# Kernel optimization log

Hardware: AMD Instinct MI355X
Metric: run time of the kernel (lower is better)

The kernel has to match this reference:

```python
import jax, jax.numpy as jnp
import numpy as np

EPS = 1e-5
NEG_SLOPE = 0.1


def conv_bn_lrelu(x, w, g, b, rm, rv):
    # 1x1 conv (no bias) + BatchNorm (inference, running stats) + LeakyReLU(0.1)
    # x: [B,C,H,W], w: [O,C]
    y = jnp.einsum('bchw,oc->bohw', x, w)
    scale = g / jnp.sqrt(rv + EPS)
    y = y * scale[None, :, None, None] + (b - rm * scale)[None, :, None, None]
    return jnp.where(y >= 0, y, NEG_SLOPE * y)


def setup_inputs() -> dict:
    key = jax.random.key(0)
    ks = jax.random.split(key, 16)
    B, C, H1, W1, H2, W2 = 4, 256, 32, 32, 64, 64
    C8 = C // 8
    inp = {
        'x1': jax.random.normal(ks[0], (B, C, H1, W1), jnp.float32),
        'x2': jax.random.normal(ks[1], (B, C, H2, W2), jnp.float32),
        'wq': jax.random.normal(ks[2], (C8, C), jnp.float32) * 0.05,
        'wk': jax.random.normal(ks[3], (C8, C), jnp.float32) * 0.05,
        'wv': jax.random.normal(ks[4], (C, C), jnp.float32) * 0.05,
        'gq': jnp.ones((C8,), jnp.float32), 'bq': jnp.zeros((C8,), jnp.float32),
        'mq': jax.random.normal(ks[5], (C8,), jnp.float32) * 0.1,
        'vq': jax.random.uniform(ks[6], (C8,), jnp.float32, 0.5, 1.5),
        'gk': jnp.ones((C8,), jnp.float32), 'bk': jnp.zeros((C8,), jnp.float32),
        'mk': jax.random.normal(ks[7], (C8,), jnp.float32) * 0.1,
        'vk': jax.random.uniform(ks[8], (C8,), jnp.float32, 0.5, 1.5),
        'gv': jnp.ones((C,), jnp.float32), 'bv': jnp.zeros((C,), jnp.float32),
        'mv': jax.random.normal(ks[9], (C,), jnp.float32) * 0.1,
        'vv': jax.random.uniform(ks[10], (C,), jnp.float32, 0.5, 1.5),
        'gamma': jnp.full((1,), 0.5, jnp.float32),
    }
    return inp


def reference(x1, x2, wq, wk, wv, gq, bq, mq, vq, gk, bk, mk, vk, gv, bv, mv, vv, gamma):
    B, C, H2, W2 = x2.shape
    # bilinear upsample x1 to x2's spatial size (align_corners=False == half-pixel)
    x1u = jax.image.resize(x1, (B, C, H2, W2), method='bilinear')
    N = H2 * W2
    q = conv_bn_lrelu(x1u, wq, gq, bq, mq, vq).reshape(B, -1, N)  # [B,C8,N]
    k = conv_bn_lrelu(x2, wk, gk, bk, mk, vk).reshape(B, -1, N)   # [B,C8,N]
    v = conv_bn_lrelu(x2, wv, gv, bv, mv, vv).reshape(B, -1, N)   # [B,C,N]
    energy = jnp.einsum('bdm,bdn->bmn', q, k)                      # [B,N,N]
    attn = jax.nn.softmax(energy, axis=-1)
    out = jnp.einsum('bcn,bmn->bcm', v, attn).reshape(B, C, H2, W2)
    return gamma[0] * out + x1u
```

## Files before the change

kernel.cpp:

```cpp
#include <hip/hip_runtime.h>

#define B_ 4
#define C_ 256
#define N_ 4096
#define LOG2E 1.4426950408889634f

typedef short short8 __attribute__((ext_vector_type(8)));
typedef short short4_ __attribute__((ext_vector_type(4)));
typedef float float4v __attribute__((ext_vector_type(4)));
typedef unsigned int uint2v __attribute__((ext_vector_type(2)));
typedef unsigned int u32;

__device__ inline unsigned short f2b(float x){
  unsigned u = __builtin_bit_cast(unsigned, x);
  u = u + 0x7FFFu + ((u >> 16) & 1u);
  return (unsigned short)(u >> 16);
}

__device__ inline u32 cvtpk(float lo, float hi){
  u32 r; asm("v_cvt_pk_bf16_f32 %0, %1, %2" : "=v"(r) : "v"(lo), "v"(hi)); return r;
}

__device__ inline void gload16(const void* g, void* l){
  __builtin_amdgcn_global_load_lds((const __attribute__((address_space(1))) u32*)g,
                                   (__attribute__((address_space(3))) u32*)l, 16, 0, 0);
}

__global__ void fold_w_kernel(const float* __restrict__ wq, const float* __restrict__ wk,
    const float* __restrict__ wv,
    const float* gq, const float* bq, const float* mq, const float* vq,
    const float* gk, const float* bk, const float* mk, const float* vk,
    const float* gv, const float* bv, const float* mv, const float* vv,
    unsigned short* wqb, unsigned short* wkb, unsigned short* wvb,
    float* biasq, float* biask, float* biasv){
  int i = blockIdx.x*256 + threadIdx.x;
  int o = i >> 8;
  float sv = gv[o]*rsqrtf(vv[o]+1e-5f);
  wvb[i] = f2b(wv[i]*sv);
  if (i < 32*256){
    int oq = i >> 8;
    float sq = gq[oq]*rsqrtf(vq[oq]+1e-5f);
    wqb[i] = f2b(wq[i]*sq*LOG2E);
    float sk = gk[oq]*rsqrtf(vk[oq]+1e-5f);
    wkb[i] = f2b(wk[i]*sk);
  }
  if (i < 256) biasv[i] = bv[i] - mv[i]*(gv[i]*rsqrtf(vv[i]+1e-5f));
  if (i < 32){
    biasq[i] = (bq[i] - mq[i]*(gq[i]*rsqrtf(vq[i]+1e-5f)))*LOG2E;
    biask[i] = bk[i] - mk[i]*(gk[i]*rsqrtf(vk[i]+1e-5f));
  }
}

__global__ __launch_bounds__(256, 2)
void pre_kernel(const float* __restrict__ x1, const float* __restrict__ x2,
                const unsigned short* __restrict__ wqb,
                const unsigned short* __restrict__ wkb,
                const unsigned short* __restrict__ wvb,
                const float* __restrict__ biasq, const float* __restrict__ biask,
                const float* __restrict__ biasv,
                float* __restrict__ x1u,
                unsigned short* __restrict__ Qb, unsigned short* __restrict__ Kb,
                unsigned short* __restrict__ Vb){
  __shared__ unsigned short xt[64*260];
  int b = blockIdx.y;
  int t = threadIdx.x;
  int lane = t&63, w = t>>6, l15 = lane&15, g = lane>>4;

  if (blockIdx.z == 0){
    int y = blockIdx.x;
    float fy = 0.5f*y - 0.25f;
    float y0f = floorf(fy); float wy = fy - y0f;
    int y0 = max(0,min(31,(int)y0f)), y1 = max(0,min(31,(int)y0f+1));
    int x = t & 63, cg = t >> 6;
    float fx = 0.5f*x - 0.25f;
    float x0f = floorf(fx); float wx = fx - x0f;
    int x0 = max(0,min(31,(int)x0f)), x1i = max(0,min(31,(int)x0f+1));
    #pragma unroll 8
    for (int i=0;i<64;i++){
      int c = cg + i*4;
      const float* s0 = x1 + ((size_t)(b*C_ + c)*32 + y0)*32;
      const float* s1 = x1 + ((size_t)(b*C_ + c)*32 + y1)*32;
      float v00=s0[x0], v01=s0[x1i], v10=s1[x0], v11=s1[x1i];
      float v0 = v00 + wx*(v01-v00), v1 = v10 + wx*(v11-v10);
      float val = v0 + wy*(v1-v0);
      x1u[(size_t)(b*C_ + c)*N_ + y*64 + x] = val;
      xt[x*260 + c] = f2b(val);
    }
    __syncthreads();
    const unsigned short* arow = xt + (w*16+l15)*260 + g*8;
    short8 a[8];
    #pragma unroll
    for (int kk=0;kk<8;kk++){
      short4_ lo = *(const short4_*)(arow + kk*32);
      short4_ hi = *(const short4_*)(arow + kk*32 + 4);
      short8 af;
      af[0]=lo[0];af[1]=lo[1];af[2]=lo[2];af[3]=lo[3];
      af[4]=hi[0];af[5]=hi[1];af[6]=hi[2];af[7]=hi[3];
      a[kk]=af;
    }
    #pragma unroll
    for (int ot=0; ot<2; ot++){
      int o = ot*16 + l15;
      const unsigned short* wrow = wqb + o*C_ + g*8;
      float4v acc = {0.f,0.f,0.f,0.f};
      #pragma unroll
      for (int kk=0;kk<8;kk++){
        short8 bf = *(const short8*)(wrow + kk*32);
        acc = __builtin_amdgcn_mfma_f32_16x16x32_bf16(a[kk], bf, acc, 0,0,0);
      }
      float bs = biasq[o];
      #pragma unroll
      for (int r=0;r<4;r++){
        float yv = acc[r] + bs;
        yv = yv >= 0.f ? yv : 0.1f*yv;
        int m = y*64 + w*16 + g*4 + r;
        Qb[(size_t)(b*N_+m)*32 + o] = f2b(yv);
      }
    }
  } else {
    int n0 = blockIdx.x*64;
    int n = t & 63, cg = t >> 6;
    #pragma unroll 8
    for (int i=0;i<64;i++){
      int c = cg + i*4;
      float v = x2[(size_t)(b*C_ + c)*N_ + n0 + n];
      xt[n*260 + c] = f2b(v);
    }
    __syncthreads();
    const unsigned short* arow = xt + (w*16+l15)*260 + g*8;
    short8 a[8];
    #pragma unroll
    for (int kk=0;kk<8;kk++){
      short4_ lo = *(const short4_*)(arow + kk*32);
      short4_ hi = *(const short4_*)(arow + kk*32 + 4);
      short8 af;
      af[0]=lo[0];af[1]=lo[1];af[2]=lo[2];af[3]=lo[3];
      af[4]=hi[0];af[5]=hi[1];af[6]=hi[2];af[7]=hi[3];
      a[kk]=af;
    }
    if (blockIdx.z == 1){
      #pragma unroll
      for (int ot=0; ot<2; ot++){
        int o = ot*16 + l15;
        const unsigned short* wrow = wkb + o*C_ + g*8;
        float4v acc = {0.f,0.f,0.f,0.f};
        #pragma unroll
        for (int kk=0;kk<8;kk++){
          short8 bf = *(const short8*)(wrow + kk*32);
          acc = __builtin_amdgcn_mfma_f32_16x16x32_bf16(a[kk], bf, acc, 0,0,0);
        }
        float bs = biask[o];
        #pragma unroll
        for (int r=0;r<4;r++){
          float yv = acc[r] + bs;
          yv = yv >= 0.f ? yv : 0.1f*yv;
          int m = n0 + w*16 + g*4 + r;
          Kb[(size_t)(b*N_+m)*32 + o] = f2b(yv);
        }
      }
    }
    int obase = (blockIdx.z == 1) ? 0 : 8;
    #pragma unroll
    for (int ot=0; ot<8; ot++){
      int o = (obase + ot)*16 + l15;
      const unsigned short* wrow = wvb + (size_t)o*C_ + g*8;
      float4v acc = {0.f,0.f,0.f,0.f};
      #pragma unroll
      for (int kk=0;kk<8;kk++){
        short8 bf = *(const short8*)(wrow + kk*32);
        acc = __builtin_amdgcn_mfma_f32_16x16x32_bf16(a[kk], bf, acc, 0,0,0);
      }
      float bs = biasv[o];
      #pragma unroll
      for (int r=0;r<4;r++){
        float yv = acc[r] + bs;
        yv = yv >= 0.f ? yv : 0.1f*yv;
        int m = n0 + w*16 + g*4 + r;
        Vb[(size_t)(b*C_ + o)*N_ + m] = f2b(yv);
      }
    }
  }
}

__global__ __launch_bounds__(512, 2)
void attn_kernel(const unsigned short* __restrict__ Qb,
                 const unsigned short* __restrict__ Kb,
                 const unsigned short* __restrict__ Vb,
                 const float* __restrict__ x1u,
                 const float* __restrict__ gamma_p,
                 float* __restrict__ out){
  __shared__ __align__(16) char smem[82720];
  int* flagsB = (int*)(smem + 81920);
  float* sclB = (float*)(smem + 81952);
  float* lst  = (float*)(smem + 82464);

  int wg = blockIdx.y*64 + blockIdx.x;
  int id = (wg & 7)*32 + (wg >> 3);
  int b = id >> 6, mblk = id & 63;
  int t = threadIdx.x, lane = t & 63, w = t >> 6;
  int l15 = lane & 15, g = lane >> 4;
  int swz = (l15 & 7) << 4;
  int cq = w & 3, ks = w >> 2;

  short8 qf{};
  if (w < 4)
    qf = *(const short8*)(Qb + (size_t)(b*N_ + mblk*64 + w*16 + l15)*32 + g*8);

  float4v acc[4][4];
  #pragma unroll
  for (int mt=0;mt<4;mt++)
    #pragma unroll
    for (int ct=0;ct<4;ct++) acc[mt][ct] = (float4v){0.f,0.f,0.f,0.f};
  float mrow = -1e30f, lrun = 0.f;
  const float4v zero4 = {0.f,0.f,0.f,0.f};

  size_t goff[4]; int loff[4];
  #pragma unroll
  for (int j=0;j<4;j++){
    int i = j*512 + t;
    int c = i >> 3, jj = i & 7;
    loff[j] = i*16;
    goff[j] = (size_t)(b*C_ + c)*(N_*2) + ((size_t)((jj ^ (c & 7)) << 4));
  }
  const char* Vbyte = (const char*)Vb;
  const short* kbase = (const short*)Kb + (size_t)(b*N_ + l15)*32 + g*8;

  auto stageV = [&](int tt, char* buf){
    const char* src = Vbyte + tt*128;
    #pragma unroll
    for (int j=0;j<4;j++) gload16(src + goff[j], buf + loff[j]);
  };
  auto loadK = [&](short8 (&kf)[4], int tt){
    const short* kp = kbase + (size_t)tt*64*32;
    #pragma unroll
    for (int j=0;j<4;j++) kf[j] = *(const short8*)(kp + j*512);
  };

  auto softmax_step = [&](const short8 (&kf)[4], int pdst){
    float4v s[4];
    #pragma unroll
    for (int j=0;j<4;j++)
      s[j] = __builtin_amdgcn_mfma_f32_16x16x32_bf16(kf[j], qf, zero4, 0, 0, 0);
    float tmax = fmaxf(fmaxf(fmaxf(s[0][0],s[0][1]),fmaxf(s[0][2],s[0][3])),
               fmaxf(fmaxf(fmaxf(s[1][0],s[1][1]),fmaxf(s[1][2],s[1][3])),
               fmaxf(fmaxf(fmaxf(s[2][0],s[2][1]),fmaxf(s[2][2],s[2][3])),
                     fmaxf(fmaxf(s[3][0],s[3][1]),fmaxf(s[3][2],s[3][3])))));
    int trig = __any((tmax > mrow + 8.f) ? 1 : 0) ? 1 : 0;
    if (lane == 0) flagsB[pdst*4 + w] = trig;
    if (trig){
      float tm = fmaxf(tmax, __shfl_xor(tmax, 16));
      tm = fmaxf(tm, __shfl_xor(tm, 32));
      float mnew = fmaxf(mrow, tm);
      float sc = exp2f(mrow - mnew);
      mrow = mnew; lrun *= sc;
      if (lane < 16) sclB[pdst*64 + w*16 + l15] = sc;
    }
    char* pw = smem + 65536 + pdst*8192 + w*2048 + l15*128;
    #pragma unroll
    for (int j=0;j<4;j++){
      float p0 = exp2f(s[j][0]-mrow), p1 = exp2f(s[j][1]-mrow);
      float p2 = exp2f(s[j][2]-mrow), p3 = exp2f(s[j][3]-mrow);
      lrun += (p0+p1)+(p2+p3);
      u32 lo = cvtpk(p0, p1);
      u32 hi = cvtpk(p2, p3);
      *(uint2v*)(pw + ((j*32 + g*8) ^ swz)) = (uint2v){lo, hi};
    }
  };

  auto body = [&](int tt, short8 (&kC)[4], short8 (&kN)[4]){
    int pp = tt & 1, vb = tt & 1;
    char* vbc = smem + vb*32768;
    if (tt < 63) stageV(tt+1, smem + (vb^1)*32768);
    if (w < 4){
      loadK(kN, (tt+2) & 63);
      if (tt < 63) softmax_step(kC, pp ^ 1);
    }
    #pragma unroll
    for (int mt=0;mt<4;mt++){
      if (flagsB[pp*4 + mt]){
        float4v sv = *(float4v*)(sclB + pp*64 + mt*16 + g*4);
        #pragma unroll
        for (int ct=0;ct<4;ct++){
          acc[mt][ct][0]*=sv[0]; acc[mt][ct][1]*=sv[1];
          acc[mt][ct][2]*=sv[2]; acc[mt][ct][3]*=sv[3];
        }
      }
    }
    int ko = (ks*64 + g*16) ^ swz;
    short8 pa[4], vf[4];
    #pragma unroll
    for (int mt=0;mt<4;mt++)
      pa[mt] = *(const short8*)(smem + 65536 + pp*8192 + mt*2048 + l15*128 + ko);
    #pragma unroll
    for (int ct=0;ct<4;ct++)
      vf[ct] = *(const short8*)(vbc + (cq*64 + ct*16 + l15)*128 + ko);
    __builtin_amdgcn_s_setprio(1);
    #pragma unroll
    for (int mt=0;mt<4;mt++)
      #pragma unroll
      for (int ct=0;ct<4;ct++)
        acc[mt][ct] = __builtin_amdgcn_mfma_f32_16x16x32_bf16(pa[mt], vf[ct], acc[mt][ct], 0, 0, 0);
    __builtin_amdgcn_s_setprio(0);
    __syncthreads();
  };

  short8 kA[4], kB[4];
  stageV(0, smem);
  if (w < 4){
    short8 k0[4];
    loadK(k0, 0);
    softmax_step(k0, 0);
    loadK(kA, 1);
  }
  __syncthreads();

  for (int tt=0; tt<64; tt+=2){
    body(tt,   kA, kB);
    body(tt+1, kB, kA);
  }

  if (w < 4){
    lrun += __shfl_xor(lrun, 16);
    lrun += __shfl_xor(lrun, 32);
    if (lane < 16) lst[w*16 + l15] = lrun;
  }
  float* cb = (float*)smem + cq*4160;
  if (ks == 1){
    #pragma unroll
    for (int mt=0;mt<4;mt++)
      #pragma unroll
      for (int ct=0;ct<4;ct++)
        #pragma unroll
        for (int r=0;r<4;r++)
          cb[(mt*16 + g*4 + r)*65 + ct*16 + l15] = acc[mt][ct][r];
  }
  __syncthreads();
  if (ks == 0){
    float4v lv[4];
    #pragma unroll
    for (int mt=0;mt<4;mt++) lv[mt] = *(float4v*)(lst + mt*16 + g*4);
    #pragma unroll
    for (int mt=0;mt<4;mt++)
      #pragma unroll
      for (int ct=0;ct<4;ct++)
        #pragma unroll
        for (int r=0;r<4;r++){
          int idx = (mt*16 + g*4 + r)*65 + ct*16 + l15;
          cb[idx] = (acc[mt][ct][r] + cb[idx]) / lv[mt][r];
        }
  }
  __syncthreads();
  float gm = gamma_p[0];
  const float* xr = x1u + (size_t)(b*C_ + cq*64 + ks*32)*N_ + mblk*64;
  float* orow = out + (size_t)(b*C_ + cq*64 + ks*32)*N_ + mblk*64;
  #pragma unroll 8
  for (int i=0; i<32; i++){
    int c_l = ks*32 + i;
    float v = cb[lane*65 + c_l];
    orow[(size_t)i*N_ + lane] = gm*v + xr[(size_t)i*N_ + lane];
  }
}

extern "C" void kernel_launch(void* const* d_in, const int* in_sizes, int n_in,
                              void* d_out, int out_size, void* d_ws, size_t ws_size,
                              hipStream_t stream){
  (void)in_sizes; (void)n_in; (void)out_size; (void)ws_size;
  const float* x1 = (const float*)d_in[0];
  const float* x2 = (const float*)d_in[1];
  const float* wq = (const float*)d_in[2];
  const float* wk = (const float*)d_in[3];
  const float* wv = (const float*)d_in[4];
  const float* gq = (const float*)d_in[5];
  const float* bq = (const float*)d_in[6];
  const float* mq = (const float*)d_in[7];
  const float* vq = (const float*)d_in[8];
  const float* gk = (const float*)d_in[9];
  const float* bk = (const float*)d_in[10];
  const float* mk = (const float*)d_in[11];
  const float* vk = (const float*)d_in[12];
  const float* gv = (const float*)d_in[13];
  const float* bv = (const float*)d_in[14];
  const float* mv = (const float*)d_in[15];
  const float* vv = (const float*)d_in[16];
  const float* gamma = (const float*)d_in[17];
  float* out = (float*)d_out;

  char* p = (char*)d_ws;
  float* x1u          = (float*)p;          p += (size_t)B_*C_*N_*4;
  unsigned short* Qb  = (unsigned short*)p; p += (size_t)B_*N_*32*2;
  unsigned short* Kb  = (unsigned short*)p; p += (size_t)B_*N_*32*2;
  unsigned short* Vb  = (unsigned short*)p; p += (size_t)B_*C_*N_*2;
  unsigned short* wqb = (unsigned short*)p; p += 32*256*2;
  unsigned short* wkb = (unsigned short*)p; p += 32*256*2;
  unsigned short* wvb = (unsigned short*)p; p += 256*256*2;
  float* biasq        = (float*)p;          p += 32*4;
  float* biask        = (float*)p;          p += 32*4;
  float* biasv        = (float*)p;          p += 256*4;

  fold_w_kernel<<<256, 256, 0, stream>>>(wq,wk,wv,gq,bq,mq,vq,gk,bk,mk,vk,gv,bv,mv,vv,
                                         wqb,wkb,wvb,biasq,biask,biasv);
  pre_kernel<<<dim3(64,4,3), 256, 0, stream>>>(x1, x2, wqb, wkb, wvb,
                                               biasq, biask, biasv, x1u, Qb, Kb, Vb);
  attn_kernel<<<dim3(64,4), 512, 0, stream>>>(Qb, Kb, Vb, x1u, gamma, out);
}
```

Before: 118.2 us.

## Single-buffer P tile, split softmax, raise attn occupancy, reshape pre_kernel grid

The attention kernel drops the double-buffered P tile in LDS. Softmax is split into a max/rescale phase before the PV MFMAs and an exp/write phase after a barrier, and an extra __syncthreads is added. This cuts LDS use so launch bounds can ask for 4 blocks per CU. The pre-kernel regroups x2 work so each block handles 32 columns and computes both K and all V channels, with z=0 blocks past 64 returning early. The extra barrier per tile and the higher register pressure from the occupancy target may offset the gains.

```diff
diff --git a/kernel.cpp b/kernel.cpp
--- a/kernel.cpp
+++ b/kernel.cpp
@@ -67,6 +67,7 @@
   int lane = t&63, w = t>>6, l15 = lane&15, g = lane>>4;
 
   if (blockIdx.z == 0){
+    if (blockIdx.x >= 64) return;
     int y = blockIdx.x;
     float fy = 0.5f*y - 0.25f;
     float y0f = floorf(fy); float wy = fy - y0f;
@@ -118,16 +119,17 @@
       }
     }
   } else {
-    int n0 = blockIdx.x*64;
-    int n = t & 63, cg = t >> 6;
+    int n0 = blockIdx.x*32;
+    int n = t & 31, cg = t >> 5;
     #pragma unroll 8
-    for (int i=0;i<64;i++){
-      int c = cg + i*4;
+    for (int i=0;i<32;i++){
+      int c = cg + i*8;
       float v = x2[(size_t)(b*C_ + c)*N_ + n0 + n];
       xt[n*260 + c] = f2b(v);
     }
     __syncthreads();
-    const unsigned short* arow = xt + (w*16+l15)*260 + g*8;
+    int mt = w & 1;
+    const unsigned short* arow = xt + (mt*16+l15)*260 + g*8;
     short8 a[8];
     #pragma unroll
     for (int kk=0;kk<8;kk++){
@@ -138,7 +140,7 @@
       af[4]=hi[0];af[5]=hi[1];af[6]=hi[2];af[7]=hi[3];
       a[kk]=af;
     }
-    if (blockIdx.z == 1){
+    if (w < 2){
       #pragma unroll
       for (int ot=0; ot<2; ot++){
         int o = ot*16 + l15;
@@ -159,10 +161,9 @@
         }
       }
     }
-    int obase = (blockIdx.z == 1) ? 0 : 8;
-    #pragma unroll
-    for (int ot=0; ot<8; ot++){
-      int o = (obase + ot)*16 + l15;
+    #pragma unroll
+    for (int i=0;i<8;i++){
+      int o = ((w>>1)*8 + i)*16 + l15;
       const unsigned short* wrow = wvb + (size_t)o*C_ + g*8;
       float4v acc = {0.f,0.f,0.f,0.f};
       #pragma unroll
@@ -175,24 +176,24 @@
       for (int r=0;r<4;r++){
         float yv = acc[r] + bs;
         yv = yv >= 0.f ? yv : 0.1f*yv;
-        int m = n0 + w*16 + g*4 + r;
+        int m = n0 + mt*16 + g*4 + r;
         Vb[(size_t)(b*C_ + o)*N_ + m] = f2b(yv);
       }
     }
   }
 }
 
-__global__ __launch_bounds__(512, 2)
+__global__ __launch_bounds__(512, 4)
 void attn_kernel(const unsigned short* __restrict__ Qb,
                  const unsigned short* __restrict__ Kb,
                  const unsigned short* __restrict__ Vb,
                  const float* __restrict__ x1u,
                  const float* __restrict__ gamma_p,
                  float* __restrict__ out){
-  __shared__ __align__(16) char smem[82720];
-  int* flagsB = (int*)(smem + 81920);
-  float* sclB = (float*)(smem + 81952);
-  float* lst  = (float*)(smem + 82464);
+  __shared__ __align__(16) char smem[74528];
+  int* flagsB = (int*)(smem + 73728);
+  float* sclB = (float*)(smem + 73760);
+  float* lst  = (float*)(smem + 74272);
 
   int wg = blockIdx.y*64 + blockIdx.x;
   int id = (wg & 7)*32 + (wg >> 3);
@@ -236,8 +237,7 @@
     for (int j=0;j<4;j++) kf[j] = *(const short8*)(kp + j*512);
   };
 
-  auto softmax_step = [&](const short8 (&kf)[4], int pdst){
-    float4v s[4];
+  auto softmaxA = [&](const short8 (&kf)[4], int pdst, float4v (&s)[4]){
     #pragma unroll
     for (int j=0;j<4;j++)
       s[j] = __builtin_amdgcn_mfma_f32_16x16x32_bf16(kf[j], qf, zero4, 0, 0, 0);
@@ -255,7 +255,9 @@
       mrow = mnew; lrun *= sc;
       if (lane < 16) sclB[pdst*64 + w*16 + l15] = sc;
     }
-    char* pw = smem + 65536 + pdst*8192 + w*2048 + l15*128;
+  };
+  auto softmaxB = [&](float4v (&s)[4]){
+    char* pw = smem + 65536 + w*2048 + l15*128;
     #pragma unroll
     for (int j=0;j<4;j++){
       float p0 = exp2f(s[j][0]-mrow), p1 = exp2f(s[j][1]-mrow);
@@ -267,13 +269,12 @@
     }
   };
 
-  auto body = [&](int tt, short8 (&kC)[4], short8 (&kN)[4]){
-    int pp = tt & 1, vb = tt & 1;
-    char* vbc = smem + vb*32768;
-    if (tt < 63) stageV(tt+1, smem + (vb^1)*32768);
+  auto body = [&](int tt, short8 (&kC)[4], short8 (&kN)[4], float4v (&s)[4]){
+    int pp = tt & 1;
+    if (tt < 63) stageV(tt+1, smem + ((tt+1)&1)*32768);
     if (w < 4){
       loadK(kN, (tt+2) & 63);
-      if (tt < 63) softmax_step(kC, pp ^ 1);
+      if (tt < 63) softmaxA(kC, (tt+1)&1, s);
     }
     #pragma unroll
     for (int mt=0;mt<4;mt++){
@@ -287,10 +288,11 @@
       }
     }
     int ko = (ks*64 + g*16) ^ swz;
+    char* vbc = smem + (tt&1)*32768;
     short8 pa[4], vf[4];
     #pragma unroll
     for (int mt=0;mt<4;mt++)
-      pa[mt] = *(const short8*)(smem + 65536 + pp*8192 + mt*2048 + l15*128 + ko);
+      pa[mt] = *(const short8*)(smem + 65536 + mt*2048 + l15*128 + ko);
     #pragma unroll
     for (int ct=0;ct<4;ct++)
       vf[ct] = *(const short8*)(vbc + (cq*64 + ct*16 + l15)*128 + ko);
@@ -302,21 +304,25 @@
         acc[mt][ct] = __builtin_amdgcn_mfma_f32_16x16x32_bf16(pa[mt], vf[ct], acc[mt][ct], 0, 0, 0);
     __builtin_amdgcn_s_setprio(0);
     __syncthreads();
+    if (w < 4 && tt < 63) softmaxB(s);
+    __syncthreads();
   };
 
   short8 kA[4], kB[4];
+  float4v sA[4], sB[4];
   stageV(0, smem);
   if (w < 4){
     short8 k0[4];
     loadK(k0, 0);
-    softmax_step(k0, 0);
+    softmaxA(k0, 0, sA);
+    softmaxB(sA);
     loadK(kA, 1);
   }
   __syncthreads();
 
   for (int tt=0; tt<64; tt+=2){
-    body(tt,   kA, kB);
-    body(tt+1, kB, kA);
+    body(tt,   kA, kB, sA);
+    body(tt+1, kB, kA, sB);
   }
 
   if (w < 4){
@@ -399,7 +405,7 @@
 
   fold_w_kernel<<<256, 256, 0, stream>>>(wq,wk,wv,gq,bq,mq,vq,gk,bk,mk,vk,gv,bv,mv,vv,
                                          wqb,wkb,wvb,biasq,biask,biasv);
-  pre_kernel<<<dim3(64,4,3), 256, 0, stream>>>(x1, x2, wqb, wkb, wvb,
-                                               biasq, biask, biasv, x1u, Qb, Kb, Vb);
+  pre_kernel<<<dim3(128,4,2), 256, 0, stream>>>(x1, x2, wqb, wkb, wvb,
+                                                biasq, biask, biasv, x1u, Qb, Kb, Vb);
   attn_kernel<<<dim3(64,4), 512, 0, stream>>>(Qb, Kb, Vb, x1u, gamma, out);
 }
```

Result: slower. 330.8 us (+179.8%).

## Triple-buffer V tiles with partial vmcnt waits instead of full syncthreads

Applied to the files above, without the earlier changes.

The V staging buffers go from double to triple buffering, and each V tile is prefetched two iterations ahead. The per-iteration __syncthreads, which drains every outstanding memory operation, is replaced by explicit s_waitcnt with partial vmcnt counts followed by a raw s_barrier, so later loads stay in flight across the barrier. Global offsets become 32-bit with a per-batch base pointer. This raises LDS use from about 82KB to about 115KB, which may cut occupancy below the 2 blocks per CU that launch_bounds asks for. It also relies on hand-counted vmcnt values that must stay in step with the compiler's load ordering.

```diff
diff --git a/kernel.cpp b/kernel.cpp
--- a/kernel.cpp
+++ b/kernel.cpp
@@ -189,10 +189,10 @@
                  const float* __restrict__ x1u,
                  const float* __restrict__ gamma_p,
                  float* __restrict__ out){
-  __shared__ __align__(16) char smem[82720];
-  int* flagsB = (int*)(smem + 81920);
-  float* sclB = (float*)(smem + 81952);
-  float* lst  = (float*)(smem + 82464);
+  __shared__ __align__(16) char smem[115488];
+  int* flagsB = (int*)(smem + 114688);
+  float* sclB = (float*)(smem + 114720);
+  float* lst  = (float*)(smem + 115232);
 
   int wg = blockIdx.y*64 + blockIdx.x;
   int id = (wg & 7)*32 + (wg >> 3);
@@ -214,19 +214,20 @@
   float mrow = -1e30f, lrun = 0.f;
   const float4v zero4 = {0.f,0.f,0.f,0.f};
 
-  size_t goff[4]; int loff[4];
+  u32 goff[4]; int loff[4];
   #pragma unroll
   for (int j=0;j<4;j++){
     int i = j*512 + t;
     int c = i >> 3, jj = i & 7;
     loff[j] = i*16;
-    goff[j] = (size_t)(b*C_ + c)*(N_*2) + ((size_t)((jj ^ (c & 7)) << 4));
-  }
-  const char* Vbyte = (const char*)Vb;
+    goff[j] = (u32)(c*(N_*2)) + (u32)((jj ^ (c & 7)) << 4);
+  }
+  const char* Vbyte = (const char*)Vb + (size_t)b*C_*N_*2;
   const short* kbase = (const short*)Kb + (size_t)(b*N_ + l15)*32 + g*8;
 
-  auto stageV = [&](int tt, char* buf){
-    const char* src = Vbyte + tt*128;
+  auto stageV = [&](int u){
+    const char* src = Vbyte + u*128;
+    char* buf = smem + (u%3)*32768;
     #pragma unroll
     for (int j=0;j<4;j++) gload16(src + goff[j], buf + loff[j]);
   };
@@ -255,7 +256,7 @@
       mrow = mnew; lrun *= sc;
       if (lane < 16) sclB[pdst*64 + w*16 + l15] = sc;
     }
-    char* pw = smem + 65536 + pdst*8192 + w*2048 + l15*128;
+    char* pw = smem + 98304 + pdst*8192 + w*2048 + l15*128;
     #pragma unroll
     for (int j=0;j<4;j++){
       float p0 = exp2f(s[j][0]-mrow), p1 = exp2f(s[j][1]-mrow);
@@ -268,9 +269,8 @@
   };
 
   auto body = [&](int tt, short8 (&kC)[4], short8 (&kN)[4]){
-    int pp = tt & 1, vb = tt & 1;
-    char* vbc = smem + vb*32768;
-    if (tt < 63) stageV(tt+1, smem + (vb^1)*32768);
+    int pp = tt & 1;
+    if (tt < 62) stageV(tt+2);
     if (w < 4){
       loadK(kN, (tt+2) & 63);
       if (tt < 63) softmax_step(kC, pp ^ 1);
@@ -287,10 +287,12 @@
       }
     }
     int ko = (ks*64 + g*16) ^ swz;
+    const char* vbc = smem + (tt%3)*32768;
+    const char* pbase = smem + 98304 + pp*8192;
     short8 pa[4], vf[4];
     #pragma unroll
     for (int mt=0;mt<4;mt++)
-      pa[mt] = *(const short8*)(smem + 65536 + pp*8192 + mt*2048 + l15*128 + ko);
+      pa[mt] = *(const short8*)(pbase + mt*2048 + l15*128 + ko);
     #pragma unroll
     for (int ct=0;ct<4;ct++)
       vf[ct] = *(const short8*)(vbc + (cq*64 + ct*16 + l15)*128 + ko);
@@ -301,18 +303,31 @@
       for (int ct=0;ct<4;ct++)
         acc[mt][ct] = __builtin_amdgcn_mfma_f32_16x16x32_bf16(pa[mt], vf[ct], acc[mt][ct], 0, 0, 0);
     __builtin_amdgcn_s_setprio(0);
-    __syncthreads();
+    if (w < 4){
+      if (tt < 62) asm volatile("s_waitcnt lgkmcnt(0) vmcnt(8)" ::: "memory");
+      else         asm volatile("s_waitcnt lgkmcnt(0) vmcnt(4)" ::: "memory");
+    } else {
+      if (tt < 62) asm volatile("s_waitcnt lgkmcnt(0) vmcnt(4)" ::: "memory");
+      else         asm volatile("s_waitcnt lgkmcnt(0) vmcnt(0)" ::: "memory");
+    }
+    __builtin_amdgcn_s_barrier();
+    __builtin_amdgcn_sched_barrier(0);
   };
 
   short8 kA[4], kB[4];
-  stageV(0, smem);
+  stageV(0);
+  stageV(1);
   if (w < 4){
     short8 k0[4];
     loadK(k0, 0);
     softmax_step(k0, 0);
     loadK(kA, 1);
-  }
-  __syncthreads();
+    asm volatile("s_waitcnt lgkmcnt(0) vmcnt(8)" ::: "memory");
+  } else {
+    asm volatile("s_waitcnt lgkmcnt(0) vmcnt(4)" ::: "memory");
+  }
+  __builtin_amdgcn_s_barrier();
+  __builtin_amdgcn_sched_barrier(0);
 
   for (int tt=0; tt<64; tt+=2){
     body(tt,   kA, kB);
```

New measurement: 143.3 us. 1.21x slower.

## Split attention over the key dimension into two halves and add a combine kernel

Applied to the files above, without the earlier changes.

The attention kernel now splits the N keys into two halves across a new grid dimension. This doubles the number of workgroups from 256 to 512 so more CUs are busy, and it shrinks LDS use. Each half writes bf16 partial outputs plus per-row max and sum statistics to workspace, and a new combine kernel rescales and merges them, applies gamma and adds the residual. The cost is an extra launch, roughly 16MB of partial-result traffic, and bf16 rounding of the partial results.

```diff
diff --git a/kernel.cpp b/kernel.cpp
--- a/kernel.cpp
+++ b/kernel.cpp
@@ -16,11 +16,12 @@
   u = u + 0x7FFFu + ((u >> 16) & 1u);
   return (unsigned short)(u >> 16);
 }
-
+__device__ inline float b2f(unsigned short s){
+  return __builtin_bit_cast(float, ((u32)s) << 16);
+}
 __device__ inline u32 cvtpk(float lo, float hi){
   u32 r; asm("v_cvt_pk_bf16_f32 %0, %1, %2" : "=v"(r) : "v"(lo), "v"(hi)); return r;
 }
-
 __device__ inline void gload16(const void* g, void* l){
   __builtin_amdgcn_global_load_lds((const __attribute__((address_space(1))) u32*)g,
                                    (__attribute__((address_space(3))) u32*)l, 16, 0, 0);
@@ -186,65 +187,59 @@
 void attn_kernel(const unsigned short* __restrict__ Qb,
                  const unsigned short* __restrict__ Kb,
                  const unsigned short* __restrict__ Vb,
-                 const float* __restrict__ x1u,
-                 const float* __restrict__ gamma_p,
-                 float* __restrict__ out){
-  __shared__ __align__(16) char smem[82720];
-  int* flagsB = (int*)(smem + 81920);
-  float* sclB = (float*)(smem + 81952);
-  float* lst  = (float*)(smem + 82464);
-
-  int wg = blockIdx.y*64 + blockIdx.x;
-  int id = (wg & 7)*32 + (wg >> 3);
-  int b = id >> 6, mblk = id & 63;
+                 unsigned short* __restrict__ partial,
+                 float* __restrict__ statsg){
+  __shared__ __align__(16) char smem[43552];
+  int* flagsB = (int*)(smem + 43008);
+  float* sclB = (float*)(smem + 43040);
+
+  int wg = (blockIdx.z*4 + blockIdx.y)*64 + blockIdx.x;
+  int id = (wg & 7)*64 + (wg >> 3);
+  int ng = id >> 8, b = (id >> 6) & 3, mblk = id & 63;
   int t = threadIdx.x, lane = t & 63, w = t >> 6;
   int l15 = lane & 15, g = lane >> 4;
-  int swz = (l15 & 7) << 4;
-  int cq = w & 3, ks = w >> 2;
 
   short8 qf{};
   if (w < 4)
     qf = *(const short8*)(Qb + (size_t)(b*N_ + mblk*64 + w*16 + l15)*32 + g*8);
 
-  float4v acc[4][4];
+  float4v acc[4][2];
   #pragma unroll
   for (int mt=0;mt<4;mt++)
     #pragma unroll
-    for (int ct=0;ct<4;ct++) acc[mt][ct] = (float4v){0.f,0.f,0.f,0.f};
+    for (int ct=0;ct<2;ct++) acc[mt][ct] = (float4v){0.f,0.f,0.f,0.f};
   float mrow = -1e30f, lrun = 0.f;
   const float4v zero4 = {0.f,0.f,0.f,0.f};
 
-  size_t goff[4]; int loff[4];
+  u32 goff[2]; int loff[2];
   #pragma unroll
-  for (int j=0;j<4;j++){
+  for (int j=0;j<2;j++){
     int i = j*512 + t;
-    int c = i >> 3, jj = i & 7;
+    int c = i >> 2, jj = i & 3;
     loff[j] = i*16;
-    goff[j] = (size_t)(b*C_ + c)*(N_*2) + ((size_t)((jj ^ (c & 7)) << 4));
-  }
-  const char* Vbyte = (const char*)Vb;
-  const short* kbase = (const short*)Kb + (size_t)(b*N_ + l15)*32 + g*8;
-
-  auto stageV = [&](int tt, char* buf){
-    const char* src = Vbyte + tt*128;
-    #pragma unroll
-    for (int j=0;j<4;j++) gload16(src + goff[j], buf + loff[j]);
+    goff[j] = (u32)(c*(N_*2)) + (u32)((jj ^ (c & 3)) << 4);
+  }
+  const char* Vbyte = (const char*)Vb + (size_t)b*C_*N_*2 + ng*4096;
+  const short* kbase = (const short*)Kb + (size_t)(b*N_ + ng*2048 + l15)*32 + g*8;
+
+  auto stageV = [&](int tt, int par){
+    const char* src = Vbyte + tt*64;
+    #pragma unroll
+    for (int j=0;j<2;j++) gload16(src + goff[j], smem + par*16384 + loff[j]);
   };
-  auto loadK = [&](short8 (&kf)[4], int tt){
-    const short* kp = kbase + (size_t)tt*64*32;
-    #pragma unroll
-    for (int j=0;j<4;j++) kf[j] = *(const short8*)(kp + j*512);
+  auto loadK = [&](short8 (&kf)[2], int tt){
+    const short* kp = kbase + (size_t)tt*1024;
+    #pragma unroll
+    for (int j=0;j<2;j++) kf[j] = *(const short8*)(kp + j*512);
   };
 
-  auto softmax_step = [&](const short8 (&kf)[4], int pdst){
-    float4v s[4];
-    #pragma unroll
-    for (int j=0;j<4;j++)
+  auto softmax_step = [&](const short8 (&kf)[2], int pdst){
+    float4v s[2];
+    #pragma unroll
+    for (int j=0;j<2;j++)
       s[j] = __builtin_amdgcn_mfma_f32_16x16x32_bf16(kf[j], qf, zero4, 0, 0, 0);
     float tmax = fmaxf(fmaxf(fmaxf(s[0][0],s[0][1]),fmaxf(s[0][2],s[0][3])),
-               fmaxf(fmaxf(fmaxf(s[1][0],s[1][1]),fmaxf(s[1][2],s[1][3])),
-               fmaxf(fmaxf(fmaxf(s[2][0],s[2][1]),fmaxf(s[2][2],s[2][3])),
-                     fmaxf(fmaxf(s[3][0],s[3][1]),fmaxf(s[3][2],s[3][3])))));
+                       fmaxf(fmaxf(s[1][0],s[1][1]),fmaxf(s[1][2],s[1][3])));
     int trig = __any((tmax > mrow + 8.f) ? 1 : 0) ? 1 : 0;
     if (lane == 0) flagsB[pdst*4 + w] = trig;
     if (trig){
@@ -255,59 +250,61 @@
       mrow = mnew; lrun *= sc;
       if (lane < 16) sclB[pdst*64 + w*16 + l15] = sc;
     }
-    char* pw = smem + 65536 + pdst*8192 + w*2048 + l15*128;
-    #pragma unroll
-    for (int j=0;j<4;j++){
+    char* pw = smem + 32768 + pdst*5120 + w*1280 + l15*80;
+    #pragma unroll
+    for (int j=0;j<2;j++){
       float p0 = exp2f(s[j][0]-mrow), p1 = exp2f(s[j][1]-mrow);
       float p2 = exp2f(s[j][2]-mrow), p3 = exp2f(s[j][3]-mrow);
       lrun += (p0+p1)+(p2+p3);
       u32 lo = cvtpk(p0, p1);
       u32 hi = cvtpk(p2, p3);
-      *(uint2v*)(pw + ((j*32 + g*8) ^ swz)) = (uint2v){lo, hi};
+      *(uint2v*)(pw + j*32 + g*8) = (uint2v){lo, hi};
     }
   };
 
-  auto body = [&](int tt, short8 (&kC)[4], short8 (&kN)[4]){
-    int pp = tt & 1, vb = tt & 1;
-    char* vbc = smem + vb*32768;
-    if (tt < 63) stageV(tt+1, smem + (vb^1)*32768);
+  auto body = [&](int tt, short8 (&kC)[2], short8 (&kN)[2]){
+    int pp = tt & 1, nx = (tt+1) & 1;
+    if (tt < 63) stageV(tt+1, nx);
     if (w < 4){
       loadK(kN, (tt+2) & 63);
-      if (tt < 63) softmax_step(kC, pp ^ 1);
+      if (tt < 63) softmax_step(kC, nx);
     }
     #pragma unroll
     for (int mt=0;mt<4;mt++){
       if (flagsB[pp*4 + mt]){
         float4v sv = *(float4v*)(sclB + pp*64 + mt*16 + g*4);
         #pragma unroll
-        for (int ct=0;ct<4;ct++){
+        for (int ct=0;ct<2;ct++){
           acc[mt][ct][0]*=sv[0]; acc[mt][ct][1]*=sv[1];
           acc[mt][ct][2]*=sv[2]; acc[mt][ct][3]*=sv[3];
         }
       }
     }
-    int ko = (ks*64 + g*16) ^ swz;
-    short8 pa[4], vf[4];
+    const char* pb = smem + 32768 + pp*5120;
+    const char* vbc = smem + pp*16384;
+    short8 pa[4], vf[2];
     #pragma unroll
     for (int mt=0;mt<4;mt++)
-      pa[mt] = *(const short8*)(smem + 65536 + pp*8192 + mt*2048 + l15*128 + ko);
-    #pragma unroll
-    for (int ct=0;ct<4;ct++)
-      vf[ct] = *(const short8*)(vbc + (cq*64 + ct*16 + l15)*128 + ko);
+      pa[mt] = *(const short8*)(pb + mt*1280 + l15*80 + g*16);
+    #pragma unroll
+    for (int ct=0;ct<2;ct++){
+      int row = w*32 + ct*16 + l15;
+      vf[ct] = *(const short8*)(vbc + row*64 + ((g*16) ^ ((row & 3) << 4)));
+    }
     __builtin_amdgcn_s_setprio(1);
     #pragma unroll
     for (int mt=0;mt<4;mt++)
       #pragma unroll
-      for (int ct=0;ct<4;ct++)
+      for (int ct=0;ct<2;ct++)
         acc[mt][ct] = __builtin_amdgcn_mfma_f32_16x16x32_bf16(pa[mt], vf[ct], acc[mt][ct], 0, 0, 0);
     __builtin_amdgcn_s_setprio(0);
     __syncthreads();
   };
 
-  short8 kA[4], kB[4];
-  stageV(0, smem);
+  short8 kA[2], kB[2];
+  stageV(0, 0);
   if (w < 4){
-    short8 k0[4];
+    short8 k0[2];
     loadK(k0, 0);
     softmax_step(k0, 0);
     loadK(kA, 1);
@@ -322,42 +319,63 @@
   if (w < 4){
     lrun += __shfl_xor(lrun, 16);
     lrun += __shfl_xor(lrun, 32);
-    if (lane < 16) lst[w*16 + l15] = lrun;
-  }
-  float* cb = (float*)smem + cq*4160;
-  if (ks == 1){
-    #pragma unroll
-    for (int mt=0;mt<4;mt++)
-      #pragma unroll
-      for (int ct=0;ct<4;ct++)
-        #pragma unroll
-        for (int r=0;r<4;r++)
-          cb[(mt*16 + g*4 + r)*65 + ct*16 + l15] = acc[mt][ct][r];
+    if (lane < 16){
+      int sidx = (((b*2+ng)*64 + mblk)*64 + w*16 + l15)*2;
+      statsg[sidx] = mrow; statsg[sidx+1] = lrun;
+    }
+  }
+  size_t pbg = (size_t)((b*2+ng)*64 + mblk)*16384;
+  #pragma unroll
+  for (int mt=0;mt<4;mt++)
+    #pragma unroll
+    for (int ct=0;ct<2;ct++)
+      #pragma unroll
+      for (int r=0;r<4;r++){
+        int m = mt*16 + g*4 + r;
+        int c = w*32 + ct*16 + l15;
+        partial[pbg + m*256 + c] = f2b(acc[mt][ct][r]);
+      }
+}
+
+__global__ __launch_bounds__(256, 2)
+void combine_kernel(const unsigned short* __restrict__ partial,
+                    const float* __restrict__ statsg,
+                    const float* __restrict__ x1u,
+                    const float* __restrict__ gamma_p,
+                    float* __restrict__ out){
+  __shared__ float tile[64][65];
+  __shared__ float fbuf[64][3];
+  int b = blockIdx.z, mblk = blockIdx.y, ct4 = blockIdx.x;
+  int t = threadIdx.x;
+  float gm = gamma_p[0];
+  if (t < 64){
+    int s0 = (((b*2+0)*64 + mblk)*64 + t)*2;
+    int s1 = (((b*2+1)*64 + mblk)*64 + t)*2;
+    float m0 = statsg[s0], l0 = statsg[s0+1];
+    float m1 = statsg[s1], l1 = statsg[s1+1];
+    float M = fmaxf(m0, m1);
+    float f0 = exp2f(m0 - M), f1 = exp2f(m1 - M);
+    float L = l0*f0 + l1*f1;
+    fbuf[t][0] = f0; fbuf[t][1] = f1; fbuf[t][2] = gm / L;
   }
   __syncthreads();
-  if (ks == 0){
-    float4v lv[4];
-    #pragma unroll
-    for (int mt=0;mt<4;mt++) lv[mt] = *(float4v*)(lst + mt*16 + g*4);
-    #pragma unroll
-    for (int mt=0;mt<4;mt++)
-      #pragma unroll
-      for (int ct=0;ct<4;ct++)
-        #pragma unroll
-        for (int r=0;r<4;r++){
-          int idx = (mt*16 + g*4 + r)*65 + ct*16 + l15;
-          cb[idx] = (acc[mt][ct][r] + cb[idx]) / lv[mt][r];
-        }
+  size_t p0b = (size_t)((b*2+0)*64 + mblk)*16384 + ct4*64;
+  size_t p1b = (size_t)((b*2+1)*64 + mblk)*16384 + ct4*64;
+  int c_l = t & 63, mg = t >> 6;
+  #pragma unroll 4
+  for (int pass=0; pass<16; pass++){
+    int m = pass*4 + mg;
+    float v0 = b2f(partial[p0b + m*256 + c_l]);
+    float v1 = b2f(partial[p1b + m*256 + c_l]);
+    tile[m][c_l] = (v0*fbuf[m][0] + v1*fbuf[m][1]) * fbuf[m][2];
   }
   __syncthreads();
-  float gm = gamma_p[0];
-  const float* xr = x1u + (size_t)(b*C_ + cq*64 + ks*32)*N_ + mblk*64;
-  float* orow = out + (size_t)(b*C_ + cq*64 + ks*32)*N_ + mblk*64;
-  #pragma unroll 8
-  for (int i=0; i<32; i++){
-    int c_l = ks*32 + i;
-    float v = cb[lane*65 + c_l];
-    orow[(size_t)i*N_ + lane] = gm*v + xr[(size_t)i*N_ + lane];
+  int m = t & 63, cg = t >> 6;
+  #pragma unroll 4
+  for (int pass=0; pass<16; pass++){
+    int c_l2 = pass*4 + cg;
+    size_t gidx = ((size_t)(b*C_ + ct4*64 + c_l2))*N_ + mblk*64 + m;
+    out[gidx] = tile[m][c_l2] + x1u[gidx];
   }
 }
 
@@ -386,20 +404,23 @@
   float* out = (float*)d_out;
 
   char* p = (char*)d_ws;
-  float* x1u          = (float*)p;          p += (size_t)B_*C_*N_*4;
-  unsigned short* Qb  = (unsigned short*)p; p += (size_t)B_*N_*32*2;
-  unsigned short* Kb  = (unsigned short*)p; p += (size_t)B_*N_*32*2;
-  unsigned short* Vb  = (unsigned short*)p; p += (size_t)B_*C_*N_*2;
-  unsigned short* wqb = (unsigned short*)p; p += 32*256*2;
-  unsigned short* wkb = (unsigned short*)p; p += 32*256*2;
-  unsigned short* wvb = (unsigned short*)p; p += 256*256*2;
-  float* biasq        = (float*)p;          p += 32*4;
-  float* biask        = (float*)p;          p += 32*4;
-  float* biasv        = (float*)p;          p += 256*4;
+  float* x1u            = (float*)p;          p += (size_t)B_*C_*N_*4;
+  unsigned short* Qb    = (unsigned short*)p; p += (size_t)B_*N_*32*2;
+  unsigned short* Kb    = (unsigned short*)p; p += (size_t)B_*N_*32*2;
+  unsigned short* Vb    = (unsigned short*)p; p += (size_t)B_*C_*N_*2;
+  unsigned short* wqb   = (unsigned short*)p; p += 32*256*2;
+  unsigned short* wkb   = (unsigned short*)p; p += 32*256*2;
+  unsigned short* wvb   = (unsigned short*)p; p += 256*256*2;
+  float* biasq          = (float*)p;          p += 32*4;
+  float* biask          = (float*)p;          p += 32*4;
+  float* biasv          = (float*)p;          p += 256*4;
+  unsigned short* parti = (unsigned short*)p; p += (size_t)512*16384*2;
+  float* statsg         = (float*)p;          p += (size_t)512*64*2*4;
 
   fold_w_kernel<<<256, 256, 0, stream>>>(wq,wk,wv,gq,bq,mq,vq,gk,bk,mk,vk,gv,bv,mv,vv,
                                          wqb,wkb,wvb,biasq,biask,biasv);
   pre_kernel<<<dim3(64,4,3), 256, 0, stream>>>(x1, x2, wqb, wkb, wvb,
                                                biasq, biask, biasv, x1u, Qb, Kb, Vb);
-  attn_kernel<<<dim3(64,4), 512, 0, stream>>>(Qb, Kb, Vb, x1u, gamma, out);
-}
+  attn_kernel<<<dim3(64,4,2), 512, 0, stream>>>(Qb, Kb, Vb, parti, statsg);
+  combine_kernel<<<dim3(4,64,4), 256, 0, stream>>>(parti, statsg, x1u, gamma, out);
+}
```

New measurement: 109.6 us, median of 4. 1.08x faster.
